# Kernel optimization log

Hardware: AMD Instinct MI355X
Metric: run time of the kernel (lower is better)

Reference implementation:

```python
import jax, jax.numpy as jnp
import numpy as np

D_MODEL = 1024
H = 16
DK = D_MODEL // H
D_FC = 4096
B = 2
S = 1024
EPS = 1e-6


def setup_inputs() -> dict:
    key = jax.random.key(0)
    ks = jax.random.split(key, 8)
    sc = 1.0 / np.sqrt(D_MODEL)
    return {
        "x": jax.random.normal(ks[0], (B, S, D_MODEL), dtype=jnp.float32),
        "mask": jnp.ones((B, 1, 1, S), dtype=jnp.int32),
        "w_q": jax.random.normal(ks[1], (D_MODEL, D_MODEL), dtype=jnp.float32) * sc,
        "w_k": jax.random.normal(ks[2], (D_MODEL, D_MODEL), dtype=jnp.float32) * sc,
        "w_v": jax.random.normal(ks[3], (D_MODEL, D_MODEL), dtype=jnp.float32) * sc,
        "w_o": jax.random.normal(ks[4], (D_MODEL, D_MODEL), dtype=jnp.float32) * sc,
        "alpha1": jnp.ones((D_MODEL,), dtype=jnp.float32),
        "beta1": jnp.zeros((D_MODEL,), dtype=jnp.float32),
        "alpha2": jnp.ones((D_MODEL,), dtype=jnp.float32),
        "beta2": jnp.zeros((D_MODEL,), dtype=jnp.float32),
        "fc1_w": jax.random.normal(ks[5], (D_FC, D_MODEL), dtype=jnp.float32) * sc,
        "fc1_b": jnp.zeros((D_FC,), dtype=jnp.float32),
        "fc2_w": jax.random.normal(ks[6], (D_MODEL, D_FC), dtype=jnp.float32) * (1.0 / np.sqrt(D_FC)),
        "fc2_b": jnp.zeros((D_MODEL,), dtype=jnp.float32),
    }


def _layernorm(x, alpha, beta):
    # Matches torch: mean and std (unbiased, ddof=1), divide by (std + eps)
    mean = jnp.mean(x, axis=-1, keepdims=True)
    std = jnp.std(x, axis=-1, keepdims=True, ddof=1)
    return alpha * (x - mean) / (std + EPS) + beta


def _mha(x, mask, w_q, w_k, w_v, w_o):
    # nn.Linear(bias=False): y = x @ W.T
    q = (x @ w_q.T).reshape(B, S, H, DK).transpose(0, 2, 1, 3)  # (B,H,S,DK)
    k = (x @ w_k.T).reshape(B, S, H, DK).transpose(0, 2, 1, 3)
    v = (x @ w_v.T).reshape(B, S, H, DK).transpose(0, 2, 1, 3)
    scores = jnp.einsum('bhqd,bhkd->bhqk', q, k) / jnp.sqrt(jnp.float32(DK))
    scores = jnp.where(mask == 0, jnp.float32(-1e9), scores)
    attn = jax.nn.softmax(scores, axis=-1)  # dropout=0 (eval)
    out = jnp.einsum('bhqk,bhkd->bhqd', attn, v)  # (B,H,S,DK)
    out = out.transpose(0, 2, 1, 3).reshape(B, S, D_MODEL)
    return out @ w_o.T


def _ffn(x, fc1_w, fc1_b, fc2_w, fc2_b):
    h = jax.nn.relu(x @ fc1_w.T + fc1_b)
    return h @ fc2_w.T + fc2_b


def reference(x, mask, w_q, w_k, w_v, w_o, alpha1, beta1, alpha2, beta2,
              fc1_w, fc1_b, fc2_w, fc2_b):
    # Pre-LN residual block 1: attention
    x = x + _mha(_layernorm(x, alpha1, beta1), mask, w_q, w_k, w_v, w_o)
    # Pre-LN residual block 2: FFN
    x = x + _ffn(_layernorm(x, alpha2, beta2), fc1_w, fc1_b, fc2_w, fc2_b)
    return x
```

## Files before the change

kernel.cpp:

```cpp
#include <hip/hip_runtime.h>
#include <hip/hip_bf16.h>


typedef __bf16 bf16;
typedef __attribute__((ext_vector_type(8))) __bf16 bf16x8;
typedef __attribute__((ext_vector_type(4))) __bf16 bf16x4;
typedef __attribute__((ext_vector_type(4))) float f32x4;
typedef __attribute__((ext_vector_type(16))) float f32x16;
typedef __attribute__((ext_vector_type(4))) unsigned int u32x4;

#define NTOK 2048
#define DM   1024
#define DFC  4096
#define QKVN 3072

__device__ inline void gl_lds16(const void* g, void* l) {
    __builtin_amdgcn_global_load_lds((const __attribute__((address_space(1))) void*)g,
                                     (__attribute__((address_space(3))) void*)l, 16, 0, 0);
}

__device__ inline unsigned cvtpk_bf16(float lo, float hi) {
    unsigned r;
    asm("v_cvt_pk_bf16_f32 %0, %1, %2" : "=v"(r) : "v"(lo), "v"(hi));
    return r;
}

__device__ inline void ln_row(float4 v, const float* alpha, const float* beta,
                              bf16* outrow, int t) {
    float s  = v.x + v.y + v.z + v.w;
    float ss = v.x * v.x + v.y * v.y + v.z * v.z + v.w * v.w;
    __shared__ float red[8];
    int lane = t & 63, wv = t >> 6;
    #pragma unroll
    for (int o = 32; o > 0; o >>= 1) {
        s  += __shfl_down(s, o);
        ss += __shfl_down(ss, o);
    }
    if (lane == 0) { red[wv] = s; red[4 + wv] = ss; }
    __syncthreads();
    float S  = red[0] + red[1] + red[2] + red[3];
    float SS = red[4] + red[5] + red[6] + red[7];
    float mean = S * (1.0f / 1024.0f);
    float var  = (SS - S * mean) * (1.0f / 1023.0f);
    var = var < 0.f ? 0.f : var;
    float inv = 1.0f / (sqrtf(var) + 1e-6f);
    float4 a4 = reinterpret_cast<const float4*>(alpha)[t];
    float4 b4 = reinterpret_cast<const float4*>(beta)[t];
    bf16x4 o4;
    o4[0] = (bf16)(a4.x * (v.x - mean) * inv + b4.x);
    o4[1] = (bf16)(a4.y * (v.y - mean) * inv + b4.y);
    o4[2] = (bf16)(a4.z * (v.z - mean) * inv + b4.z);
    o4[3] = (bf16)(a4.w * (v.w - mean) * inv + b4.w);
    reinterpret_cast<bf16x4*>(outrow)[t] = o4;
}

__global__ __launch_bounds__(256) void prep_kernel(
    const float4* __restrict__ wq, const float4* __restrict__ wk,
    const float4* __restrict__ wv, bf16x4* __restrict__ oqkv,
    const float* __restrict__ x, const float* __restrict__ alpha1,
    const float* __restrict__ beta1, bf16* __restrict__ xn) {
    int blk = blockIdx.x;
    int t = threadIdx.x;
    if (blk < 3072) {
        int i = blk * 256 + t;
        const int Q = 262144;
        float4 v = (i < Q) ? wq[i] : (i < 2 * Q) ? wk[i - Q] : wv[i - 2 * Q];
        bf16x4 o;
        o[0] = (bf16)v.x; o[1] = (bf16)v.y; o[2] = (bf16)v.z; o[3] = (bf16)v.w;
        oqkv[i] = o;
    } else {
        int row = blk - 3072;
        float4 v = reinterpret_cast<const float4*>(x + (size_t)row * DM)[t];
        ln_row(v, alpha1, beta1, xn + (size_t)row * DM, t);
    }
}

__global__ __launch_bounds__(256) void reduce_ln_kernel(const float* __restrict__ p,
                                                        const float* __restrict__ resid,
                                                        const float* __restrict__ alpha,
                                                        const float* __restrict__ beta,
                                                        float* __restrict__ x2,
                                                        bf16* __restrict__ xn) {
    int row = blockIdx.x, t = threadIdx.x;
    size_t i4 = (size_t)row * 256 + t;
    const size_t SL = 524288;
    float4 a = reinterpret_cast<const float4*>(p)[i4];
    float4 b = reinterpret_cast<const float4*>(p)[i4 + SL];
    float4 c = reinterpret_cast<const float4*>(p)[i4 + 2 * SL];
    float4 d = reinterpret_cast<const float4*>(p)[i4 + 3 * SL];
    float4 r = reinterpret_cast<const float4*>(resid)[i4];
    float4 v;
    v.x = a.x + b.x + c.x + d.x + r.x;
    v.y = a.y + b.y + c.y + d.y + r.y;
    v.z = a.z + b.z + c.z + d.z + r.z;
    v.w = a.w + b.w + c.w + d.w + r.w;
    reinterpret_cast<float4*>(x2)[i4] = v;
    ln_row(v, alpha, beta, xn + (size_t)row * DM, t);
}

__global__ __launch_bounds__(256) void reduce_out_kernel(const float* __restrict__ p,
                                                         const float* __restrict__ bias,
                                                         const float* __restrict__ x2,
                                                         float* __restrict__ out) {
    size_t i4 = (size_t)blockIdx.x * 256 + threadIdx.x;
    const size_t SL = 524288;
    float4 a = reinterpret_cast<const float4*>(p)[i4];
    float4 b = reinterpret_cast<const float4*>(p)[i4 + SL];
    float4 c = reinterpret_cast<const float4*>(p)[i4 + 2 * SL];
    float4 d = reinterpret_cast<const float4*>(p)[i4 + 3 * SL];
    float4 r = reinterpret_cast<const float4*>(x2)[i4];
    float4 bi = reinterpret_cast<const float4*>(bias)[i4 & 255];
    float4 o;
    o.x = a.x + b.x + c.x + d.x + r.x + bi.x;
    o.y = a.y + b.y + c.y + d.y + r.y + bi.y;
    o.z = a.z + b.z + c.z + d.z + r.z + bi.z;
    o.w = a.w + b.w + c.w + d.w + r.w + bi.w;
    reinterpret_cast<float4*>(out)[i4] = o;
}

template <int EPI>
__global__ __launch_bounds__(256) void gemm128(const bf16* __restrict__ A,
                                               const bf16* __restrict__ Bt,
                                               void* __restrict__ outp,
                                               bf16* __restrict__ vt,
                                               const float* __restrict__ bias,
                                               int M, int N, int K, int kslice,
                                               int nbx, int nby) {
    __shared__ bf16 As[2][128 * 64];
    __shared__ bf16 Bs[2][128 * 64];
    int tid = threadIdx.x;
    int lane = tid & 63, wave = tid >> 6;
    int q = lane >> 4, r = lane & 15;
    int wm = wave >> 1, wn = wave & 1;

    int lid = blockIdx.y * nbx + blockIdx.x;
    int nxp = nbx >> 3;
    int xcd = lid & 7;
    int loc = lid >> 3;
    int bx = xcd * nxp + (loc % nxp);
    int by = loc / nxp;

    int m0 = by * 128, n0 = bx * 128;
    int kbeg = blockIdx.z * kslice;
    int nit = kslice / 64;
    f32x4 acc[4][4] = {};

    int srow = tid >> 3;
    int csrc = (tid & 7) ^ (srow & 7);
    const bf16* agp = A  + (size_t)(m0 + srow) * K + kbeg + csrc * 8;
    const bf16* bgp = Bt + (size_t)(n0 + srow) * K + kbeg + csrc * 8;

    int co0 = ((q ^ (r & 7)) * 8);
    int co1 = co0 ^ 32;
    int aoff = (wm * 64 + r) * 64;
    int boff = (wn * 64 + r) * 64;

    auto stage = [&](int it, int b) {
        int k0 = it * 64;
        #pragma unroll
        for (int j = 0; j < 4; ++j) {
            gl_lds16(agp + (size_t)j * 32 * K + k0, &As[b][tid * 8 + j * 2048]);
            gl_lds16(bgp + (size_t)j * 32 * K + k0, &Bs[b][tid * 8 + j * 2048]);
        }
    };

    stage(0, 0);
    for (int it = 0; it < nit; ++it) {
        __syncthreads();
        if (it + 1 < nit) stage(it + 1, (it + 1) & 1);
        const bf16* Ab = &As[it & 1][aoff];
        const bf16* Bb = &Bs[it & 1][boff];
        #pragma unroll
        for (int half = 0; half < 2; ++half) {
            int co = half ? co1 : co0;
            bf16x8 af[4], bfv[4];
            #pragma unroll
            for (int t = 0; t < 4; ++t)
                af[t] = *reinterpret_cast<const bf16x8*>(Ab + t * 1024 + co);
            #pragma unroll
            for (int u = 0; u < 4; ++u)
                bfv[u] = *reinterpret_cast<const bf16x8*>(Bb + u * 1024 + co);
            #pragma unroll
            for (int t = 0; t < 4; ++t)
                #pragma unroll
                for (int u = 0; u < 4; ++u)
                    acc[t][u] = __builtin_amdgcn_mfma_f32_16x16x32_bf16(af[t], bfv[u], acc[t][u], 0, 0, 0);
        }
    }

    if (EPI == 2 && n0 >= 2048) {
        int bb = m0 >> 10;
        int sb = (m0 & 1023) + wm * 64 + q * 4;
        int vrow0 = bb * 1024 + (n0 - 2048) + wn * 64;
        #pragma unroll
        for (int t = 0; t < 4; ++t) {
            #pragma unroll
            for (int u = 0; u < 4; ++u) {
                bf16x4 pk;
                #pragma unroll
                for (int i = 0; i < 4; ++i) pk[i] = (bf16)acc[t][u][i];
                *reinterpret_cast<bf16x4*>(vt + (size_t)(vrow0 + u * 16 + r) * 1024 + sb + t * 16) = pk;
            }
        }
        return;
    }

    size_t zoff = (size_t)blockIdx.z * M * N;
    #pragma unroll
    for (int t = 0; t < 4; ++t) {
        #pragma unroll
        for (int u = 0; u < 4; ++u) {
            #pragma unroll
            for (int i = 0; i < 4; ++i) {
                int mm = m0 + wm * 64 + t * 16 + q * 4 + i;
                int nn = n0 + wn * 64 + u * 16 + r;
                size_t idx = (size_t)mm * N + nn;
                float v = acc[t][u][i];
                if (EPI == 1) {
                    v += bias[nn];
                    ((bf16*)outp)[idx] = (bf16)(v > 0.f ? v : 0.f);
                } else if (EPI == 2) {
                    ((bf16*)outp)[idx] = (bf16)v;
                } else {
                    ((float*)outp)[zoff + idx] = v;
                }
            }
        }
    }
}

__global__ __launch_bounds__(256) void attn_kernel(const bf16* __restrict__ qkv,
                                                   const bf16* __restrict__ Vt,
                                                   const int* __restrict__ mask,
                                                   bf16* __restrict__ out,
                                                   const float4* __restrict__ cwo,
                                                   const float4* __restrict__ cf1,
                                                   const float4* __restrict__ cf2,
                                                   bf16x4* __restrict__ oo,
                                                   bf16x4* __restrict__ of1,
                                                   bf16x4* __restrict__ of2) {
    __shared__ bf16 Ks[2][4096];
    __shared__ bf16 Vs[2][4096];
    __shared__ float msk[1024];
    __shared__ float als[4][32];
    int tid = threadIdx.x;

    if (blockIdx.x >= 256) {
        int base = (blockIdx.x - 256) * 1024;
        const int Q = 262144;
        #pragma unroll
        for (int k = 0; k < 4; ++k) {
            int i = base + k * 256 + tid;
            float4 v;
            bf16x4* dst;
            if (i < Q)          { v = cwo[i];         dst = oo  + i; }
            else if (i < 5 * Q) { v = cf1[i - Q];     dst = of1 + (i - Q); }
            else                { v = cf2[i - 5 * Q]; dst = of2 + (i - 5 * Q); }
            bf16x4 o;
            o[0] = (bf16)v.x; o[1] = (bf16)v.y; o[2] = (bf16)v.z; o[3] = (bf16)v.w;
            *dst = o;
        }
        return;
    }

    int lane = tid & 63, w = tid >> 6;
    int l5 = lane & 31, hi = lane >> 5;

    int id = blockIdx.x;
    int xcd = id & 7, jj = id >> 3;
    int bh = xcd * 4 + (jj >> 3);
    int qb = jj & 7;
    int b = bh >> 4, h = bh & 15;

    {
        int4 mi = reinterpret_cast<const int4*>(mask + b * 1024)[tid];
        msk[tid * 4 + 0] = mi.x ? 0.f : -1e9f;
        msk[tid * 4 + 1] = mi.y ? 0.f : -1e9f;
        msk[tid * 4 + 2] = mi.z ? 0.f : -1e9f;
        msk[tid * 4 + 3] = mi.w ? 0.f : -1e9f;
    }

    int qrow0 = qb * 128 + w * 32;
    const bf16* qp = qkv + (size_t)(b * 1024 + qrow0 + l5) * QKVN + h * 64 + hi * 8;
    bf16x8 qf[4];
    #pragma unroll
    for (int ks = 0; ks < 4; ++ks)
        qf[ks] = *reinterpret_cast<const bf16x8*>(qp + ks * 16);

    int csw = (tid & 7) ^ ((tid >> 3) & 7);
    const bf16* kg0 = qkv + (size_t)(b * 1024 + (tid >> 3)) * QKVN + 1024 + h * 64 + csw * 8;
    const bf16* kg1 = kg0 + (size_t)32 * QKVN;
    const bf16* vg0 = Vt + (size_t)((b * 16 + h) * 64 + (tid >> 3)) * 1024 + csw * 8;
    const bf16* vg1 = vg0 + 32 * 1024;
    bf16* kld = &Ks[0][tid * 8];
    bf16* vld = &Vs[0][tid * 8];

    gl_lds16(kg0, kld);
    gl_lds16(kg1, kld + 2048);
    gl_lds16(vg0, vld);
    gl_lds16(vg1, vld + 2048);

    float m_run = -1e30f, l_half = 0.f;
    f32x16 o0 = {};
    f32x16 o1 = {};

    for (int t = 0; t < 16; ++t) {
        __syncthreads();
        if (t < 15) {
            int ktn = (t + 1) * 64;
            int bo = ((t + 1) & 1) * 4096;
            gl_lds16(kg0 + (size_t)ktn * QKVN, kld + bo);
            gl_lds16(kg1 + (size_t)ktn * QKVN, kld + bo + 2048);
            gl_lds16(vg0 + ktn, vld + bo);
            gl_lds16(vg1 + ktn, vld + bo + 2048);
        }
        const bf16* Kb = Ks[t & 1];
        const bf16* Vb = Vs[t & 1];
        int kt = t * 64;

        f32x16 s0 = {}, s1 = {};
        __builtin_amdgcn_s_setprio(1);
        #pragma unroll
        for (int ks = 0; ks < 4; ++ks) {
            int ch = (((ks << 1) + hi) ^ (l5 & 7)) << 3;
            bf16x8 k0 = *reinterpret_cast<const bf16x8*>(&Kb[l5 * 64 + ch]);
            bf16x8 k1 = *reinterpret_cast<const bf16x8*>(&Kb[(32 + l5) * 64 + ch]);
            s0 = __builtin_amdgcn_mfma_f32_32x32x16_bf16(k0, qf[ks], s0, 0, 0, 0);
            s1 = __builtin_amdgcn_mfma_f32_32x32x16_bf16(k1, qf[ks], s1, 0, 0, 0);
        }
        __builtin_amdgcn_s_setprio(0);

        float p0[16], p1[16];
        float pmax = -1e30f;
        #pragma unroll
        for (int g = 0; g < 4; ++g) {
            float4 mb0 = *reinterpret_cast<const float4*>(&msk[kt + g * 8 + hi * 4]);
            float4 mb1 = *reinterpret_cast<const float4*>(&msk[kt + 32 + g * 8 + hi * 4]);
            #pragma unroll
            for (int i = 0; i < 4; ++i) {
                float mbv0 = (i == 0) ? mb0.x : (i == 1) ? mb0.y : (i == 2) ? mb0.z : mb0.w;
                float mbv1 = (i == 0) ? mb1.x : (i == 1) ? mb1.y : (i == 2) ? mb1.z : mb1.w;
                float a0 = fmaf(s0[g * 4 + i], 0.125f, mbv0);
                float a1 = fmaf(s1[g * 4 + i], 0.125f, mbv1);
                p0[g * 4 + i] = a0;
                p1[g * 4 + i] = a1;
                pmax = fmaxf(pmax, fmaxf(a0, a1));
            }
        }
        pmax = fmaxf(pmax, __shfl_xor(pmax, 32));
        float mnew = fmaxf(m_run, pmax);
        if (!__all(pmax - m_run <= 8.0f)) {
            float alpha = __expf(m_run - mnew);
            m_run = mnew;
            l_half *= alpha;
            als[w][l5] = alpha;
            #pragma unroll
            for (int g = 0; g < 4; ++g) {
                float4 av = *reinterpret_cast<const float4*>(&als[w][g * 8 + hi * 4]);
                o0[g * 4 + 0] *= av.x; o0[g * 4 + 1] *= av.y;
                o0[g * 4 + 2] *= av.z; o0[g * 4 + 3] *= av.w;
                o1[g * 4 + 0] *= av.x; o1[g * 4 + 1] *= av.y;
                o1[g * 4 + 2] *= av.z; o1[g * 4 + 3] *= av.w;
            }
        }
        float sum = 0.f;
        #pragma unroll
        for (int rg = 0; rg < 16; ++rg) {
            p0[rg] = __expf(p0[rg] - m_run);
            p1[rg] = __expf(p1[rg] - m_run);
            sum += p0[rg] + p1[rg];
        }
        l_half += sum;

        __builtin_amdgcn_s_setprio(1);
        #pragma unroll
        for (int tile = 0; tile < 2; ++tile) {
            const float* pp = tile ? p1 : p0;
            #pragma unroll
            for (int kp = 0; kp < 2; ++kp) {
                unsigned uA0 = cvtpk_bf16(pp[8 * kp + 0], pp[8 * kp + 1]);
                unsigned uA1 = cvtpk_bf16(pp[8 * kp + 2], pp[8 * kp + 3]);
                unsigned uB0 = cvtpk_bf16(pp[8 * kp + 4], pp[8 * kp + 5]);
                unsigned uB1 = cvtpk_bf16(pp[8 * kp + 6], pp[8 * kp + 7]);
                unsigned us0 = hi ? uB0 : uA0, us1 = hi ? uB1 : uA1;
                unsigned ug0 = hi ? uA0 : uB0, ug1 = hi ? uA1 : uB1;
                unsigned r0 = (unsigned)__shfl_xor((int)ug0, 32);
                unsigned r1 = (unsigned)__shfl_xor((int)ug1, 32);
                u32x4 pw_;
                pw_[0] = hi ? r0 : us0;
                pw_[1] = hi ? r1 : us1;
                pw_[2] = hi ? us0 : r0;
                pw_[3] = hi ? us1 : r1;
                bf16x8 pf = *reinterpret_cast<bf16x8*>(&pw_);
                int vch = (((tile << 2) + (kp << 1) + hi) ^ (l5 & 7)) << 3;
                bf16x8 v0 = *reinterpret_cast<const bf16x8*>(&Vb[l5 * 64 + vch]);
                bf16x8 v1 = *reinterpret_cast<const bf16x8*>(&Vb[(32 + l5) * 64 + vch]);
                o0 = __builtin_amdgcn_mfma_f32_32x32x16_bf16(pf, v0, o0, 0, 0, 0);
                o1 = __builtin_amdgcn_mfma_f32_32x32x16_bf16(pf, v1, o1, 0, 0, 0);
            }
        }
        __builtin_amdgcn_s_setprio(0);
    }

    float l_tot = l_half + __shfl_xor(l_half, 32);
    als[w][l5] = 1.0f / l_tot;
    bf16* ob = out + (size_t)(b * 1024 + qrow0) * DM + h * 64;
    #pragma unroll
    for (int g = 0; g < 4; ++g) {
        float4 iv = *reinterpret_cast<const float4*>(&als[w][g * 8 + hi * 4]);
        #pragma unroll
        for (int i = 0; i < 4; ++i) {
            float ivv = (i == 0) ? iv.x : (i == 1) ? iv.y : (i == 2) ? iv.z : iv.w;
            int qr = g * 8 + hi * 4 + i;
            ob[(size_t)qr * DM + l5]      = (bf16)(o0[g * 4 + i] * ivv);
            ob[(size_t)qr * DM + 32 + l5] = (bf16)(o1[g * 4 + i] * ivv);
        }
    }
}

extern "C" void kernel_launch(void* const* d_in, const int* in_sizes, int n_in,
                              void* d_out, int out_size, void* d_ws, size_t ws_size,
                              hipStream_t stream) {
    const float* x      = (const float*)d_in[0];
    const int*   mask   = (const int*)  d_in[1];
    const float* w_q    = (const float*)d_in[2];
    const float* w_k    = (const float*)d_in[3];
    const float* w_v    = (const float*)d_in[4];
    const float* w_o    = (const float*)d_in[5];
    const float* alpha1 = (const float*)d_in[6];
    const float* beta1  = (const float*)d_in[7];
    const float* alpha2 = (const float*)d_in[8];
    const float* beta2  = (const float*)d_in[9];
    const float* fc1_w  = (const float*)d_in[10];
    const float* fc1_b  = (const float*)d_in[11];
    const float* fc2_w  = (const float*)d_in[12];
    const float* fc2_b  = (const float*)d_in[13];
    float* out = (float*)d_out;

    char* ws = (char*)d_ws;
    const size_t MB = 1024 * 1024;
    bf16*  wqkv_b = (bf16*)(ws +  0 * MB);
    bf16*  wo_b   = (bf16*)(ws +  6 * MB);
    bf16*  f1w_b  = (bf16*)(ws +  8 * MB);
    bf16*  f2w_b  = (bf16*)(ws + 16 * MB);
    bf16*  xn     = (bf16*)(ws + 24 * MB);
    bf16*  qkvb   = (bf16*)(ws + 28 * MB);
    bf16*  vtb    = (bf16*)(ws + 40 * MB);
    bf16*  attnb  = (bf16*)(ws + 44 * MB);
    float* x2     = (float*)(ws + 48 * MB);
    float* po     = (float*)(ws + 56 * MB);
    bf16*  hb     = (bf16*)(ws + 28 * MB);
    float* pf2    = (float*)(ws + 56 * MB);

    prep_kernel<<<5120, 256, 0, stream>>>(
        (const float4*)w_q, (const float4*)w_k, (const float4*)w_v,
        (bf16x4*)wqkv_b, x, alpha1, beta1, xn);

    gemm128<2><<<dim3(24, 16, 1), 256, 0, stream>>>(
        xn, wqkv_b, qkvb, vtb, nullptr, NTOK, QKVN, DM, DM, 24, 16);

    attn_kernel<<<2560, 256, 0, stream>>>(
        qkvb, vtb, mask, attnb,
        (const float4*)w_o, (const float4*)fc1_w, (const float4*)fc2_w,
        (bf16x4*)wo_b, (bf16x4*)f1w_b, (bf16x4*)f2w_b);

    gemm128<4><<<dim3(8, 16, 4), 256, 0, stream>>>(
        attnb, wo_b, po, nullptr, nullptr, NTOK, DM, DM, DM / 4, 8, 16);

    reduce_ln_kernel<<<NTOK, 256, 0, stream>>>(po, x, alpha2, beta2, x2, xn);

    gemm128<1><<<dim3(32, 16, 1), 256, 0, stream>>>(
        xn, f1w_b, hb, nullptr, fc1_b, NTOK, DFC, DM, DM, 32, 16);

    gemm128<4><<<dim3(8, 16, 4), 256, 0, stream>>>(
        hb, f2w_b, pf2, nullptr, nullptr, NTOK, DM, DFC, DFC / 4, 8, 16);

    reduce_out_kernel<<<2048, 256, 0, stream>>>(pf2, fc2_b, x2, out);
}
```

Baseline: 239.3 us.

## Add triple-buffered 128x256 GEMM with 512 threads for FFN layers

```diff
diff --git a/kernel.cpp b/kernel.cpp
--- a/kernel.cpp
+++ b/kernel.cpp
@@ -123,7 +123,6 @@
                                                const bf16* __restrict__ Bt,
                                                void* __restrict__ outp,
                                                bf16* __restrict__ vt,
-                                               const float* __restrict__ bias,
                                                int M, int N, int K, int kslice,
                                                int nbx, int nby) {
     __shared__ bf16 As[2][128 * 64];
@@ -216,11 +215,123 @@
                 int nn = n0 + wn * 64 + u * 16 + r;
                 size_t idx = (size_t)mm * N + nn;
                 float v = acc[t][u][i];
+                if (EPI == 2) {
+                    ((bf16*)outp)[idx] = (bf16)v;
+                } else {
+                    ((float*)outp)[zoff + idx] = v;
+                }
+            }
+        }
+    }
+}
+
+template <int EPI>
+__global__ __launch_bounds__(512) void gemm_3buf(const bf16* __restrict__ A,
+                                                 const bf16* __restrict__ Bt,
+                                                 void* __restrict__ outp,
+                                                 const float* __restrict__ bias,
+                                                 int M, int N, int K, int kslice,
+                                                 int nbx, int nby) {
+    __shared__ bf16 As[3][128 * 64];
+    __shared__ bf16 Bs[3][256 * 64];
+    int tid = threadIdx.x;
+    int lane = tid & 63, wave = tid >> 6;
+    int q = lane >> 4, r = lane & 15;
+    int wm = wave >> 2, wn = wave & 3;
+
+    int bx, by;
+    if (nbx >= 8) {
+        int lid = blockIdx.y * nbx + blockIdx.x;
+        int nxp = nbx >> 3;
+        int xcd = lid & 7;
+        int loc = lid >> 3;
+        bx = xcd * nxp + (loc % nxp);
+        by = loc / nxp;
+    } else {
+        bx = blockIdx.x; by = blockIdx.y;
+    }
+
+    int m0 = by * 128, n0 = bx * 256;
+    int kbeg = blockIdx.z * kslice;
+    int nt = kslice / 64;
+    f32x4 acc[4][4] = {};
+
+    int srow = tid >> 3;
+    int csrc = (tid & 7) ^ (srow & 7);
+    const bf16* agp = A  + (size_t)(m0 + srow) * K + kbeg + csrc * 8;
+    const bf16* bgp = Bt + (size_t)(n0 + srow) * K + kbeg + csrc * 8;
+
+    int co0 = ((q ^ (r & 7)) * 8);
+    int aoff = (wm * 64 + r) * 64;
+    int boff = (wn * 64 + r) * 64;
+
+    auto stage_p0 = [&](int it, int b) {
+        int k0 = it * 64;
+        gl_lds16(agp + k0,                  &As[b][tid * 8]);
+        gl_lds16(agp + (size_t)64 * K + k0, &As[b][4096 + tid * 8]);
+        gl_lds16(bgp + k0,                  &Bs[b][tid * 8]);
+    };
+    auto stage_p1 = [&](int it, int b) {
+        int k0 = it * 64;
+        gl_lds16(bgp + (size_t)64 * K + k0,  &Bs[b][4096 + tid * 8]);
+        gl_lds16(bgp + (size_t)128 * K + k0, &Bs[b][8192 + tid * 8]);
+        gl_lds16(bgp + (size_t)192 * K + k0, &Bs[b][12288 + tid * 8]);
+    };
+
+    stage_p0(0, 0); stage_p1(0, 0);
+    stage_p0(1, 1); stage_p1(1, 1);
+    asm volatile("s_waitcnt vmcnt(6)" ::: "memory");
+    __builtin_amdgcn_s_barrier();
+
+    for (int t = 0; t < nt; ++t) {
+        const bf16* Ab = &As[t % 3][aoff];
+        const bf16* Bb = &Bs[t % 3][boff];
+        bool pf = (t + 2) < nt;
+        int nb = (t + 2) % 3;
+        #pragma unroll
+        for (int ph = 0; ph < 2; ++ph) {
+            int co = co0 ^ (ph * 32);
+            bf16x8 af[4], bfv[4];
+            #pragma unroll
+            for (int tt = 0; tt < 4; ++tt)
+                af[tt] = *reinterpret_cast<const bf16x8*>(Ab + tt * 1024 + co);
+            #pragma unroll
+            for (int u = 0; u < 4; ++u)
+                bfv[u] = *reinterpret_cast<const bf16x8*>(Bb + u * 1024 + co);
+            if (pf) {
+                if (ph == 0) stage_p0(t + 2, nb);
+                else         stage_p1(t + 2, nb);
+            }
+            __builtin_amdgcn_s_setprio(1);
+            #pragma unroll
+            for (int tt = 0; tt < 4; ++tt)
+                #pragma unroll
+                for (int u = 0; u < 4; ++u)
+                    acc[tt][u] = __builtin_amdgcn_mfma_f32_16x16x32_bf16(
+                        af[tt], bfv[u], acc[tt][u], 0, 0, 0);
+            __builtin_amdgcn_s_setprio(0);
+        }
+        if (t + 1 < nt) {
+            if (pf) asm volatile("s_waitcnt vmcnt(6)" ::: "memory");
+            else    asm volatile("s_waitcnt vmcnt(0)" ::: "memory");
+            __builtin_amdgcn_s_barrier();
+        }
+    }
+
+    size_t zoff = (size_t)blockIdx.z * M * N;
+    #pragma unroll
+    for (int tt = 0; tt < 4; ++tt) {
+        #pragma unroll
+        for (int u = 0; u < 4; ++u) {
+            #pragma unroll
+            for (int i = 0; i < 4; ++i) {
+                int mm = m0 + wm * 64 + tt * 16 + q * 4 + i;
+                int nn = n0 + wn * 64 + u * 16 + r;
+                size_t idx = (size_t)mm * N + nn;
+                float v = acc[tt][u][i];
                 if (EPI == 1) {
                     v += bias[nn];
                     ((bf16*)outp)[idx] = (bf16)(v > 0.f ? v : 0.f);
-                } else if (EPI == 2) {
-                    ((bf16*)outp)[idx] = (bf16)v;
                 } else {
                     ((float*)outp)[zoff + idx] = v;
                 }
@@ -457,7 +568,7 @@
         (bf16x4*)wqkv_b, x, alpha1, beta1, xn);
 
     gemm128<2><<<dim3(24, 16, 1), 256, 0, stream>>>(
-        xn, wqkv_b, qkvb, vtb, nullptr, NTOK, QKVN, DM, DM, 24, 16);
+        xn, wqkv_b, qkvb, vtb, NTOK, QKVN, DM, DM, 24, 16);
 
     attn_kernel<<<2560, 256, 0, stream>>>(
         qkvb, vtb, mask, attnb,
@@ -465,15 +576,15 @@
         (bf16x4*)wo_b, (bf16x4*)f1w_b, (bf16x4*)f2w_b);
 
     gemm128<4><<<dim3(8, 16, 4), 256, 0, stream>>>(
-        attnb, wo_b, po, nullptr, nullptr, NTOK, DM, DM, DM / 4, 8, 16);
+        attnb, wo_b, po, nullptr, NTOK, DM, DM, DM / 4, 8, 16);
 
     reduce_ln_kernel<<<NTOK, 256, 0, stream>>>(po, x, alpha2, beta2, x2, xn);
 
-    gemm128<1><<<dim3(32, 16, 1), 256, 0, stream>>>(
-        xn, f1w_b, hb, nullptr, fc1_b, NTOK, DFC, DM, DM, 32, 16);
-
-    gemm128<4><<<dim3(8, 16, 4), 256, 0, stream>>>(
-        hb, f2w_b, pf2, nullptr, nullptr, NTOK, DM, DFC, DFC / 4, 8, 16);
+    gemm_3buf<1><<<dim3(16, 16, 1), 512, 0, stream>>>(
+        xn, f1w_b, hb, fc1_b, NTOK, DFC, DM, DM, 16, 16);
+
+    gemm_3buf<4><<<dim3(4, 16, 4), 512, 0, stream>>>(
+        hb, f2w_b, pf2, nullptr, NTOK, DM, DFC, DFC / 4, 4, 16);
 
     reduce_out_kernel<<<2048, 256, 0, stream>>>(pf2, fc2_b, x2, out);
 }
```

Result: no change. 236.7 us, median of 2 (-1.1%).
